# Performance work log

Measured on AMD Instinct MI355X. Metric: run time of the kernel, lower is better.

The kernel has to match this reference:

```python
import jax, jax.numpy as jnp
import numpy as np

CASCADING_LOSS = 0.85


def _bilinear_sample(img, px, py):
    """grid_sample(align_corners=True, padding_mode='zeros') in pixel coords.
    img: [B,C,H,W]; px,py: [B,H,W] absolute pixel coordinates."""
    B, C, H, W = img.shape
    x0 = jnp.floor(px)
    y0 = jnp.floor(py)
    x1 = x0 + 1.0
    y1 = y0 + 1.0
    wx1 = px - x0
    wx0 = 1.0 - wx1
    wy1 = py - y0
    wy0 = 1.0 - wy1

    def gather(yi, xi):
        valid = (xi >= 0) & (xi <= W - 1) & (yi >= 0) & (yi <= H - 1)
        xc = jnp.clip(xi, 0, W - 1).astype(jnp.int32)
        yc = jnp.clip(yi, 0, H - 1).astype(jnp.int32)
        # per-batch advanced indexing: [B,C,H,W]
        vals = jax.vmap(lambda im, yy, xx: im[:, yy, xx])(img, yc, xc)
        return vals * valid[:, None, :, :].astype(img.dtype)

    out = (gather(y0, x0) * (wy0 * wx0)[:, None, :, :]
           + gather(y0, x1) * (wy0 * wx1)[:, None, :, :]
           + gather(y1, x0) * (wy1 * wx0)[:, None, :, :]
           + gather(y1, x1) * (wy1 * wx1)[:, None, :, :])
    return out


def _add_flow(img, flw):
    # img: [B,C,H,W]; flw: [B,2,H,W] with channel 0 -> y offset, channel 1 -> x offset
    B, C, H, W = img.shape
    base_x = jnp.arange(W, dtype=img.dtype)[None, None, :]   # [1,1,W]
    base_y = jnp.arange(H, dtype=img.dtype)[None, :, None]   # [1,H,1]
    px = base_x + flw[:, 1, :, :]
    py = base_y + flw[:, 0, :, :]
    return _bilinear_sample(img, px, py)


def _compute_psnr(target, estim):
    mse = jnp.mean((target - estim) ** 2)
    return 10.0 * jnp.log(1.0 / mse) / jnp.log(jnp.asarray(10.0, target.dtype))


def setup_inputs() -> dict:
    key = jax.random.key(0)
    k1, k2, k3 = jax.random.split(key, 3)
    ITERS, B, H, W, C = 12, 4, 384, 512, 3
    flow_tup = jax.random.normal(k1, (ITERS, B, 2, H, W), dtype=jnp.float32)
    frame1 = jax.random.uniform(k2, (B, C, H, W), dtype=jnp.float32)
    frame2 = jax.random.uniform(k3, (B, C, H, W), dtype=jnp.float32)
    return {"flow_tup": flow_tup, "frame1": frame1, "frame2": frame2}


def reference(flow_tup, frame1, frame2):
    n_iters = flow_tup.shape[0]
    # vectorize warp over GRU iterations
    estims = jax.vmap(lambda f: _add_flow(frame1, f))(flow_tup)  # [I,B,C,H,W]
    psnrs = jax.vmap(lambda e: _compute_psnr(frame2, e))(estims)  # [I]
    weights = CASCADING_LOSS ** (n_iters - jnp.arange(n_iters, dtype=flow_tup.dtype))
    loss = -jnp.sum(psnrs * weights)
    return loss
```

## Files before the change

### kernel.cpp

```cpp
#include <hip/hip_runtime.h>
#include <math.h>

typedef _Float16 h2 __attribute__((ext_vector_type(2)));

static __device__ __forceinline__ h2 pkrtz(float a, float b) {
    return __builtin_bit_cast(h2, __builtin_amdgcn_cvt_pkrtz(a, b));
}
static __device__ __forceinline__ float getc(float4 v, int j) {
    switch (j) { case 0: return v.x; case 1: return v.y; case 2: return v.z; default: return v.w; }
}

#define ITERS 12
#define BATCH 4
#define CH 3
#define H 384
#define W 512

constexpr int HW  = H * W;
constexpr int CHW = CH * HW;
constexpr int TILE_X = 32, TILE_Y = 32;
constexpr int TX_N = W / TILE_X;
constexpr int TY_N = H / TILE_Y;
constexpr int NBLK = BATCH * TX_N * TY_N;
constexpr int HALO = 8;
constexpr int WIN_W = TILE_X + 2 * HALO;
constexpr int WIN_H = TILE_Y + 2 * HALO;
constexpr int WIN_CELLS = WIN_W * WIN_H;
constexpr int FSTRIDE = BATCH * 2 * HW;

template <bool INTERIOR>
static __device__ __forceinline__ float tap_px(
    const uint2* __restrict__ win, int xg, float yf, float fx, float fy,
    int x_t, int y_t, h2 t01, h2 t2p)
{
    float pxf = (float)xg + fx;
    float pyf = yf + fy;
    float x0f = floorf(pxf), y0f = floorf(pyf);
    float wx1 = pxf - x0f, wy1 = pyf - y0f;
    float wx0 = 1.0f - wx1, wy0 = 1.0f - wy1;
    int x0 = (int)x0f, y0 = (int)y0f;

    float w00 = wy0 * wx0;
    float w01 = wy0 * wx1;
    float w10 = wy1 * wx0;
    float w11 = wy1 * wx1;

    if (!INTERIOR) {
        int x1 = x0 + 1, y1 = y0 + 1;
        bool vx0 = (x0 >= 0) & (x0 <= W - 1);
        bool vx1 = (x1 >= 0) & (x1 <= W - 1);
        bool vy0 = (y0 >= 0) & (y0 <= H - 1);
        bool vy1 = (y1 >= 0) & (y1 <= H - 1);
        w00 *= (float)(vy0 && vx0);
        w01 *= (float)(vy0 && vx1);
        w10 *= (float)(vy1 && vx0);
        w11 *= (float)(vy1 && vx1);
    }

    int a = (y0 - (y_t - HALO)) * WIN_W + (x0 - (x_t - HALO));
    a = min(max(a, 0), WIN_CELLS - WIN_W - 2);

    uint2 c00 = win[a];
    uint2 c10 = win[a + WIN_W];
    uint2 c01 = win[a + 1];
    uint2 c11 = win[a + WIN_W + 1];

    h2 w00h = pkrtz(w00, w00);
    h2 w01h = pkrtz(w01, w01);
    h2 w10h = pkrtz(w10, w10);
    h2 w11h = pkrtz(w11, w11);

    h2 v01 = __builtin_bit_cast(h2, c00.x) * w00h
           + __builtin_bit_cast(h2, c01.x) * w01h
           + __builtin_bit_cast(h2, c10.x) * w10h
           + __builtin_bit_cast(h2, c11.x) * w11h;
    h2 v2  = __builtin_bit_cast(h2, c00.y) * w00h
           + __builtin_bit_cast(h2, c01.y) * w01h
           + __builtin_bit_cast(h2, c10.y) * w10h
           + __builtin_bit_cast(h2, c11.y) * w11h;

    h2 d01 = t01 - v01;
    h2 d2  = t2p - v2;
    return (float)d01.x * (float)d01.x + (float)d01.y * (float)d01.y
         + (float)d2.x * (float)d2.x;
}

__global__ __launch_bounds__(256, 6) void warp_mse_kernel(
    const float* __restrict__ flow,
    const float* __restrict__ f1,
    const float* __restrict__ f2,
    float* __restrict__ partials)
{
    __shared__ uint2 win[WIN_CELLS];

    int tid = threadIdx.x;
    int bx  = blockIdx.x;
    int b   = bx / (TX_N * TY_N);
    int t   = bx - b * (TX_N * TY_N);
    int ty  = t / TX_N;
    int tx  = t - ty * TX_N;
    int x_t = tx * TILE_X, y_t = ty * TILE_Y;
    bool interior = (tx > 0) & (tx < TX_N - 1) & (ty > 0) & (ty < TY_N - 1);

    const float* f1b = f1 + b * CHW;
    const float* f2b = f2 + b * CHW;

    for (int q = tid; q < (WIN_W / 2) * WIN_H; q += 256) {
        int row = q / (WIN_W / 2);
        int cp  = q - row * (WIN_W / 2);
        int gx0 = x_t - HALO + 2 * cp;
        int gxc = min(max(gx0, 0), W - 2);
        int gy  = min(max(y_t - HALO + row, 0), H - 1);
        const float* src = f1b + gy * W + gxc;
        float2 c0 = *(const float2*)(src);
        float2 c1 = *(const float2*)(src + HW);
        float2 c2 = *(const float2*)(src + 2 * HW);
        unsigned a0 = __builtin_bit_cast(unsigned, pkrtz(c0.x, c1.x));
        unsigned b0 = __builtin_bit_cast(unsigned, pkrtz(c2.x, 0.0f));
        unsigned a1 = __builtin_bit_cast(unsigned, pkrtz(c0.y, c1.y));
        unsigned b1 = __builtin_bit_cast(unsigned, pkrtz(c2.y, 0.0f));
        int wb = row * WIN_W + 2 * cp;
        win[wb]     = make_uint2(a0, b0);
        win[wb + 1] = make_uint2(a1, b1);
    }
    __syncthreads();

    int x = x_t + 4 * (tid & 7);
    int y = y_t + (tid >> 3);
    int p = y * W + x;
    float yf = (float)y;

    float4 tc0 = *(const float4*)(f2b + p);
    float4 tc1 = *(const float4*)(f2b + HW + p);
    float4 tc2 = *(const float4*)(f2b + 2 * HW + p);
    h2 t01[4], t2p[4];
#pragma unroll
    for (int j = 0; j < 4; ++j) {
        t01[j] = pkrtz(getc(tc0, j), getc(tc1, j));
        t2p[j] = pkrtz(getc(tc2, j), 0.0f);
    }

    alignas(16) float acc[ITERS];
#pragma unroll
    for (int k = 0; k < ITERS; ++k) acc[k] = 0.0f;

    const float* fp = flow + b * 2 * HW + p;
    float4 fyq[3], fxq[3];
#pragma unroll
    for (int k = 0; k < 3; ++k) {
        fyq[k] = *(const float4*)(fp + k * FSTRIDE);
        fxq[k] = *(const float4*)(fp + k * FSTRIDE + HW);
    }

#pragma unroll
    for (int it = 0; it < ITERS; ++it) {
        const float* fp3 = fp + 3 * FSTRIDE;
        float4 fyn = make_float4(0.f, 0.f, 0.f, 0.f), fxn = fyn;
        if (it + 3 < ITERS) { fyn = *(const float4*)(fp3); fxn = *(const float4*)(fp3 + HW); }

        float a_it = 0.0f;
        if (interior) {
#pragma unroll
            for (int j = 0; j < 4; ++j)
                a_it += tap_px<true >(win, x + j, yf, getc(fxq[0], j), getc(fyq[0], j),
                                      x_t, y_t, t01[j], t2p[j]);
        } else {
#pragma unroll
            for (int j = 0; j < 4; ++j)
                a_it += tap_px<false>(win, x + j, yf, getc(fxq[0], j), getc(fyq[0], j),
                                      x_t, y_t, t01[j], t2p[j]);
        }
        acc[it] = a_it;
        fyq[0] = fyq[1]; fxq[0] = fxq[1];
        fyq[1] = fyq[2]; fxq[1] = fxq[2];
        fyq[2] = fyn;    fxq[2] = fxn;
        fp += FSTRIDE;
    }

    __syncthreads();
    float* scr = (float*)win;
    float4* sc4 = (float4*)scr;
    const float4* av = (const float4*)acc;
    sc4[tid * 3 + 0] = av[0];
    sc4[tid * 3 + 1] = av[1];
    sc4[tid * 3 + 2] = av[2];
    __syncthreads();

    int lane = tid & 63;
    int wv   = tid >> 6;
#pragma unroll
    for (int r = 0; r < 3; ++r) {
        int k = wv + 4 * r;
        float s = scr[lane * 12 + k]
                + scr[(lane + 64) * 12 + k]
                + scr[(lane + 128) * 12 + k]
                + scr[(lane + 192) * 12 + k];
#pragma unroll
        for (int off = 32; off > 0; off >>= 1)
            s += __shfl_down(s, off, 64);
        if (lane == 0) partials[k * NBLK + bx] = s;
    }
}

__global__ __launch_bounds__(768) void finalize_kernel(
    const float* __restrict__ partials,
    float* __restrict__ out)
{
    __shared__ float psnr_w[ITERS];
    int wave = threadIdx.x >> 6;
    int lane = threadIdx.x & 63;

    float s = 0.0f;
    const float* pp = partials + wave * NBLK;
    for (int j = lane; j < NBLK; j += 64)
        s += pp[j];
#pragma unroll
    for (int off = 32; off > 0; off >>= 1)
        s += __shfl_down(s, off, 64);

    if (lane == 0) {
        float mse  = s * (1.0f / (float)(BATCH * CH * HW));
        float psnr = -10.0f * 0.30102999566398f * log2f(mse);
        float w = 1.0f;
        for (int k = 0; k < ITERS - wave; ++k) w *= 0.85f;
        psnr_w[wave] = psnr * w;
    }
    __syncthreads();
    if (threadIdx.x == 0) {
        float loss = 0.0f;
#pragma unroll
        for (int i = 0; i < ITERS; ++i) loss += psnr_w[i];
        out[0] = -loss;
    }
}

extern "C" void kernel_launch(void* const* d_in, const int* in_sizes, int n_in,
                              void* d_out, int out_size, void* d_ws, size_t ws_size,
                              hipStream_t stream) {
    const float* flow = (const float*)d_in[0];
    const float* f1   = (const float*)d_in[1];
    const float* f2   = (const float*)d_in[2];
    float* out        = (float*)d_out;
    float* partials   = (float*)d_ws;

    warp_mse_kernel<<<NBLK, 256, 0, stream>>>(flow, f1, f2, partials);
    finalize_kernel<<<1, 768, 0, stream>>>(partials, out);
}
```

Measured before the change: 138.0 us.

## Halve tile height, duplicate shifted LDS window for 128-bit neighbor pair loads

Shrinks the tile to 32x16 so each thread handles 2 pixels instead of 4, doubling the block count and raising the occupancy hint to 8. The LDS window is stored twice, once as-is and once shifted by one cell, so each bilinear sample reads two 16-byte LDS loads instead of four 8-byte ones. Flow loads use nontemporal hints. The gains are fewer LDS instructions and more parallelism, paid for with double LDS footprint, more halo reloading per block, and extra stores when building the window.

```diff
diff --git a/kernel.cpp b/kernel.cpp
--- a/kernel.cpp
+++ b/kernel.cpp
@@ -2,12 +2,14 @@
 #include <math.h>
 
 typedef _Float16 h2 __attribute__((ext_vector_type(2)));
+typedef float    f2 __attribute__((ext_vector_type(2)));
 
 static __device__ __forceinline__ h2 pkrtz(float a, float b) {
     return __builtin_bit_cast(h2, __builtin_amdgcn_cvt_pkrtz(a, b));
 }
-static __device__ __forceinline__ float getc(float4 v, int j) {
-    switch (j) { case 0: return v.x; case 1: return v.y; case 2: return v.z; default: return v.w; }
+static __device__ __forceinline__ float2 ldnt2(const float* p) {
+    f2 v = __builtin_nontemporal_load((const f2*)p);
+    return make_float2(v.x, v.y);
 }
 
 #define ITERS 12
@@ -18,7 +20,7 @@
 
 constexpr int HW  = H * W;
 constexpr int CHW = CH * HW;
-constexpr int TILE_X = 32, TILE_Y = 32;
+constexpr int TILE_X = 32, TILE_Y = 16;
 constexpr int TX_N = W / TILE_X;
 constexpr int TY_N = H / TILE_Y;
 constexpr int NBLK = BATCH * TX_N * TY_N;
@@ -30,7 +32,8 @@
 
 template <bool INTERIOR>
 static __device__ __forceinline__ float tap_px(
-    const uint2* __restrict__ win, int xg, float yf, float fx, float fy,
+    const uint4* __restrict__ winA4, const uint4* __restrict__ winB4,
+    int xg, float yf, float fx, float fy,
     int x_t, int y_t, h2 t01, h2 t2p)
 {
     float pxf = (float)xg + fx;
@@ -60,24 +63,24 @@
     int a = (y0 - (y_t - HALO)) * WIN_W + (x0 - (x_t - HALO));
     a = min(max(a, 0), WIN_CELLS - WIN_W - 2);
 
-    uint2 c00 = win[a];
-    uint2 c10 = win[a + WIN_W];
-    uint2 c01 = win[a + 1];
-    uint2 c11 = win[a + WIN_W + 1];
+    int k = a >> 1;
+    const uint4* w4 = (a & 1) ? winB4 : winA4;
+    uint4 r0 = w4[k];
+    uint4 r1 = w4[k + WIN_W / 2];
 
     h2 w00h = pkrtz(w00, w00);
     h2 w01h = pkrtz(w01, w01);
     h2 w10h = pkrtz(w10, w10);
     h2 w11h = pkrtz(w11, w11);
 
-    h2 v01 = __builtin_bit_cast(h2, c00.x) * w00h
-           + __builtin_bit_cast(h2, c01.x) * w01h
-           + __builtin_bit_cast(h2, c10.x) * w10h
-           + __builtin_bit_cast(h2, c11.x) * w11h;
-    h2 v2  = __builtin_bit_cast(h2, c00.y) * w00h
-           + __builtin_bit_cast(h2, c01.y) * w01h
-           + __builtin_bit_cast(h2, c10.y) * w10h
-           + __builtin_bit_cast(h2, c11.y) * w11h;
+    h2 v01 = __builtin_bit_cast(h2, r0.x) * w00h
+           + __builtin_bit_cast(h2, r0.z) * w01h
+           + __builtin_bit_cast(h2, r1.x) * w10h
+           + __builtin_bit_cast(h2, r1.z) * w11h;
+    h2 v2  = __builtin_bit_cast(h2, r0.y) * w00h
+           + __builtin_bit_cast(h2, r0.w) * w01h
+           + __builtin_bit_cast(h2, r1.y) * w10h
+           + __builtin_bit_cast(h2, r1.w) * w11h;
 
     h2 d01 = t01 - v01;
     h2 d2  = t2p - v2;
@@ -85,13 +88,14 @@
          + (float)d2.x * (float)d2.x;
 }
 
-__global__ __launch_bounds__(256, 6) void warp_mse_kernel(
+__global__ __launch_bounds__(256, 8) void warp_mse_kernel(
     const float* __restrict__ flow,
     const float* __restrict__ f1,
     const float* __restrict__ f2,
     float* __restrict__ partials)
 {
-    __shared__ uint2 win[WIN_CELLS];
+    __shared__ alignas(16) uint2 winA[WIN_CELLS];
+    __shared__ alignas(16) uint2 winB[WIN_CELLS];
 
     int tid = threadIdx.x;
     int bx  = blockIdx.x;
@@ -105,7 +109,9 @@
     const float* f1b = f1 + b * CHW;
     const float* f2b = f2 + b * CHW;
 
-    for (int q = tid; q < (WIN_W / 2) * WIN_H; q += 256) {
+#pragma unroll
+    for (int k = 0; k < 3; ++k) {
+        int q   = tid + 256 * k;
         int row = q / (WIN_W / 2);
         int cp  = q - row * (WIN_W / 2);
         int gx0 = x_t - HALO + 2 * cp;
@@ -120,55 +126,52 @@
         unsigned a1 = __builtin_bit_cast(unsigned, pkrtz(c0.y, c1.y));
         unsigned b1 = __builtin_bit_cast(unsigned, pkrtz(c2.y, 0.0f));
         int wb = row * WIN_W + 2 * cp;
-        win[wb]     = make_uint2(a0, b0);
-        win[wb + 1] = make_uint2(a1, b1);
-    }
-    __syncthreads();
-
-    int x = x_t + 4 * (tid & 7);
-    int y = y_t + (tid >> 3);
+        uint2 V0 = make_uint2(a0, b0), V1 = make_uint2(a1, b1);
+        *(uint4*)&winA[wb] = make_uint4(V0.x, V0.y, V1.x, V1.y);
+        winB[wb] = V1;
+        winB[(wb == 0) ? (WIN_CELLS - 1) : (wb - 1)] = V0;
+    }
+    __syncthreads();
+
+    int x = x_t + 2 * (tid & 15);
+    int y = y_t + (tid >> 4);
     int p = y * W + x;
     float yf = (float)y;
 
-    float4 tc0 = *(const float4*)(f2b + p);
-    float4 tc1 = *(const float4*)(f2b + HW + p);
-    float4 tc2 = *(const float4*)(f2b + 2 * HW + p);
-    h2 t01[4], t2p[4];
-#pragma unroll
-    for (int j = 0; j < 4; ++j) {
-        t01[j] = pkrtz(getc(tc0, j), getc(tc1, j));
-        t2p[j] = pkrtz(getc(tc2, j), 0.0f);
-    }
+    float2 tc0 = *(const float2*)(f2b + p);
+    float2 tc1 = *(const float2*)(f2b + HW + p);
+    float2 tc2 = *(const float2*)(f2b + 2 * HW + p);
+    h2 t01a = pkrtz(tc0.x, tc1.x), t2pa = pkrtz(tc2.x, 0.0f);
+    h2 t01b = pkrtz(tc0.y, tc1.y), t2pb = pkrtz(tc2.y, 0.0f);
 
     alignas(16) float acc[ITERS];
 #pragma unroll
     for (int k = 0; k < ITERS; ++k) acc[k] = 0.0f;
 
     const float* fp = flow + b * 2 * HW + p;
-    float4 fyq[3], fxq[3];
+    float2 fyq[3], fxq[3];
 #pragma unroll
     for (int k = 0; k < 3; ++k) {
-        fyq[k] = *(const float4*)(fp + k * FSTRIDE);
-        fxq[k] = *(const float4*)(fp + k * FSTRIDE + HW);
-    }
+        fyq[k] = ldnt2(fp + k * FSTRIDE);
+        fxq[k] = ldnt2(fp + k * FSTRIDE + HW);
+    }
+
+    const uint4* winA4 = (const uint4*)winA;
+    const uint4* winB4 = (const uint4*)winB;
 
 #pragma unroll
     for (int it = 0; it < ITERS; ++it) {
         const float* fp3 = fp + 3 * FSTRIDE;
-        float4 fyn = make_float4(0.f, 0.f, 0.f, 0.f), fxn = fyn;
-        if (it + 3 < ITERS) { fyn = *(const float4*)(fp3); fxn = *(const float4*)(fp3 + HW); }
-
-        float a_it = 0.0f;
+        float2 fyn = make_float2(0.f, 0.f), fxn = fyn;
+        if (it + 3 < ITERS) { fyn = ldnt2(fp3); fxn = ldnt2(fp3 + HW); }
+
+        float a_it;
         if (interior) {
-#pragma unroll
-            for (int j = 0; j < 4; ++j)
-                a_it += tap_px<true >(win, x + j, yf, getc(fxq[0], j), getc(fyq[0], j),
-                                      x_t, y_t, t01[j], t2p[j]);
+            a_it = tap_px<true >(winA4, winB4, x,     yf, fxq[0].x, fyq[0].x, x_t, y_t, t01a, t2pa)
+                 + tap_px<true >(winA4, winB4, x + 1, yf, fxq[0].y, fyq[0].y, x_t, y_t, t01b, t2pb);
         } else {
-#pragma unroll
-            for (int j = 0; j < 4; ++j)
-                a_it += tap_px<false>(win, x + j, yf, getc(fxq[0], j), getc(fyq[0], j),
-                                      x_t, y_t, t01[j], t2p[j]);
+            a_it = tap_px<false>(winA4, winB4, x,     yf, fxq[0].x, fyq[0].x, x_t, y_t, t01a, t2pa)
+                 + tap_px<false>(winA4, winB4, x + 1, yf, fxq[0].y, fyq[0].y, x_t, y_t, t01b, t2pb);
         }
         acc[it] = a_it;
         fyq[0] = fyq[1]; fxq[0] = fxq[1];
@@ -178,7 +181,7 @@
     }
 
     __syncthreads();
-    float* scr = (float*)win;
+    float* scr = (float*)winA;
     float4* sc4 = (float4*)scr;
     const float4* av = (const float4*)acc;
     sc4[tid * 3 + 0] = av[0];
```

Measured after the change: 135.5 us. About the same (-1.8%).
